# Kernel optimization log

Hardware: AMD Instinct MI355X
Metric: run time of the kernel (lower is better)

## Reference

```python
import jax, jax.numpy as jnp
import numpy as np

N = 50000          # nodes
DEG = 16           # uniform neighbor count (avg_degree)
IN_CH = 128        # node feature dim
TYPE_DIM = 32      # type embedding dim
NUM_TYPES = 8
OUT_CH = 128
F = IN_CH + TYPE_DIM   # SAGEConv input dim = 160
H = F                  # PyG LSTMAggregation: LSTM(in_channels, in_channels)


def setup_inputs() -> dict:
    key = jax.random.key(0)
    ks = jax.random.split(key, 12)
    x = jax.random.normal(ks[0], (N, IN_CH), dtype=jnp.float32)
    node_type_ids = jax.random.randint(ks[1], (N,), 0, NUM_TYPES)
    # each node is destination of exactly DEG edges; dst sorted (PyG lstm aggr requires sorted index)
    dst = jnp.repeat(jnp.arange(N), DEG)
    src = jax.random.randint(ks[2], (N * DEG,), 0, N)
    edge_index = jnp.stack([src, dst])
    emb_table = jax.random.normal(ks[3], (NUM_TYPES, TYPE_DIM), dtype=jnp.float32)
    s = 1.0 / np.sqrt(H)
    W_ih = jax.random.uniform(ks[4], (4 * H, F), minval=-s, maxval=s, dtype=jnp.float32)
    W_hh = jax.random.uniform(ks[5], (4 * H, H), minval=-s, maxval=s, dtype=jnp.float32)
    b_ih = jax.random.uniform(ks[6], (4 * H,), minval=-s, maxval=s, dtype=jnp.float32)
    b_hh = jax.random.uniform(ks[7], (4 * H,), minval=-s, maxval=s, dtype=jnp.float32)
    W_l = jax.random.normal(ks[8], (OUT_CH, F), dtype=jnp.float32) * 0.05  # lin_l (with bias)
    b_l = jnp.zeros((OUT_CH,), jnp.float32)
    W_r = jax.random.normal(ks[9], (OUT_CH, F), dtype=jnp.float32) * 0.05  # lin_r (root, no bias)
    return dict(x=x, node_type_ids=node_type_ids, edge_index=edge_index,
                emb_table=emb_table, W_ih=W_ih, W_hh=W_hh, b_ih=b_ih, b_hh=b_hh,
                W_l=W_l, b_l=b_l, W_r=W_r)


def reference(x, node_type_ids, edge_index, emb_table, W_ih, W_hh, b_ih, b_hh, W_l, b_l, W_r):
    n = x.shape[0]
    # type embedding lookup + concat
    h_in = jnp.concatenate([x, emb_table[node_type_ids]], axis=1)   # [N, F]
    src, dst = edge_index[0], edge_index[1]                          # dst sorted
    E = src.shape[0]
    # dense-batch the neighbor messages per destination (to_dense_batch)
    counts = jax.ops.segment_sum(jnp.ones((E,), jnp.int32), dst, num_segments=n)
    starts = jnp.concatenate([jnp.zeros((1,), jnp.int32), jnp.cumsum(counts)[:-1].astype(jnp.int32)])
    pos = jnp.arange(E, dtype=jnp.int32) - starts[dst]               # slot within each node's row
    dense = jnp.zeros((n, DEG, F), h_in.dtype).at[dst, pos].set(h_in[src])  # [N, DEG, F]

    # LSTM aggregation over neighbor sequence (PyG takes last time-step output)
    def step(carry, x_t):
        hh, cc = carry
        gates = x_t @ W_ih.T + b_ih + hh @ W_hh.T + b_hh
        i, f, g, o = jnp.split(gates, 4, axis=-1)
        cc = jax.nn.sigmoid(f) * cc + jax.nn.sigmoid(i) * jnp.tanh(g)
        hh = jax.nn.sigmoid(o) * jnp.tanh(cc)
        return (hh, cc), None

    h0 = jnp.zeros((n, H), h_in.dtype)
    (h_last, _), _ = jax.lax.scan(step, (h0, h0), dense.transpose(1, 0, 2))  # scan over DEG steps

    # SAGEConv: lin_l(aggregated) + lin_r(root), then ReLU (dropout = identity in eval)
    out = h_last @ W_l.T + b_l + h_in @ W_r.T
    return jax.nn.relu(out)
```

## Files before the change

### kernel.cpp

```cpp
#include <hip/hip_runtime.h>
#include <hip/hip_bf16.h>

#define N_NODES 50000
#define DEG     16
#define IN_CH   128
#define TYPE_DIM 32
#define F_DIM   160
#define H_DIM   160
#define OUT_CH  128
#define NSTEP   16
#define LS      168
#define NRES    7

typedef short  bf16x8 __attribute__((ext_vector_type(8)));
typedef float  f32x4  __attribute__((ext_vector_type(4)));
typedef unsigned int u32x4 __attribute__((ext_vector_type(4)));

__device__ ushort g_hin[N_NODES * F_DIM];
__device__ ushort g_wfrag[400 * 64 * 8];
__device__ ushort g_wlrfrag[80 * 64 * 8];
__device__ float  g_bsum[4 * H_DIM];

static __device__ __forceinline__ ushort f2bf(float v) {
    union { float f; unsigned u; } x; x.f = v;
    unsigned r = x.u + 0x7fff + ((x.u >> 16) & 1);
    return (ushort)(r >> 16);
}
static __device__ __forceinline__ float sigmoid_fast(float x) {
    return __builtin_amdgcn_rcpf(1.f + __expf(-x));
}
static __device__ __forceinline__ float tanh_fast(float x) {
    float e = __expf(2.f * x);
    return 1.f - 2.f * __builtin_amdgcn_rcpf(e + 1.f);
}

__global__ void pack_kernel(const float* __restrict__ Wih, const float* __restrict__ Whh,
                            const float* __restrict__ bih, const float* __restrict__ bhh,
                            const float* __restrict__ Wl,  const float* __restrict__ Wr)
{
    int gid = blockIdx.x * 256 + threadIdx.x;
    if (gid < 400 * 64) {
        int frag = gid >> 6, lane = gid & 63;
        int p = frag & 3, kc = (frag >> 2) % 10, qg = frag / 40;
        int row = p * 160 + qg * 16 + (lane & 15);
        int quad = lane >> 4;
        const float* src; int k0;
        if (kc < 5) { src = Wih + row * 160; k0 = kc * 32 + quad * 8; }
        else        { src = Whh + row * 160; k0 = (kc - 5) * 32 + quad * 8; }
        ushort tmp[8];
        #pragma unroll
        for (int j = 0; j < 8; j++) tmp[j] = f2bf(src[k0 + j]);
        ((u32x4*)g_wfrag)[frag * 64 + lane] = *(const u32x4*)tmp;
    } else if (gid < 400 * 64 + 80 * 64) {
        int g2 = gid - 400 * 64;
        int frag = g2 >> 6, lane = g2 & 63;
        int nt = frag & 7, kc = frag >> 3;
        int row = nt * 16 + (lane & 15);
        int quad = lane >> 4;
        int k0 = kc * 32 + quad * 8;
        ushort tmp[8];
        #pragma unroll
        for (int j = 0; j < 8; j++) {
            int k = k0 + j;
            float v = (k < 160) ? Wl[row * 160 + k] : Wr[row * 160 + (k - 160)];
            tmp[j] = f2bf(v);
        }
        ((u32x4*)g_wlrfrag)[frag * 64 + lane] = *(const u32x4*)tmp;
    } else if (gid < 400 * 64 + 80 * 64 + 640) {
        int i = gid - (400 * 64 + 80 * 64);
        g_bsum[i] = bih[i] + bhh[i];
    }
}

__global__ void build_hin(const float* __restrict__ x, const int* __restrict__ tids,
                          const float* __restrict__ emb)
{
    int i = blockIdx.x * 256 + threadIdx.x;
    if (i >= N_NODES * F_DIM) return;
    int n = i / F_DIM, d = i - n * F_DIM;
    float v = (d < IN_CH) ? x[n * IN_CH + d] : emb[tids[n] * TYPE_DIM + (d - IN_CH)];
    g_hin[i] = f2bf(v);
}

__launch_bounds__(640, 3)
__global__ void lstm_sage_db(const int* __restrict__ edge_src,
                             const float* __restrict__ bl,
                             float* __restrict__ out)
{
    extern __shared__ ushort lds[];
    constexpr int BSZ  = 64 * LS;
    constexpr int XOFF = 0;
    constexpr int HOFF = 2 * BSZ;
    constexpr int WOFF = 4 * BSZ;

    const int tid  = threadIdx.x;
    const int lane = tid & 63;
    const int wv   = tid >> 6;
    const int col  = lane & 15, quad = lane >> 4;
    const int nb   = blockIdx.x * 64;

    float bG4[4];
    #pragma unroll
    for (int p = 0; p < 4; p++) bG4[p] = g_bsum[p * 160 + wv * 16 + col];

    for (int i = tid; i < BSZ; i += 640) lds[HOFF + i] = 0;

    float c_st[4][4];
    #pragma unroll
    for (int m = 0; m < 4; m++)
        #pragma unroll
        for (int r = 0; r < 4; r++) c_st[m][r] = 0.f;

    const int grow  = tid / 10;
    const int gpart = tid - grow * 10;
    const int node_g = nb + grow;
    const int own = (node_g < N_NODES ? node_g : 0);
    const int sbase = own * DEG;

    const u32x4* wq = (const u32x4*)g_wfrag + wv * 40 * 64 + lane;

    {
        u32x4* wl = (u32x4*)(lds + WOFF) + wv * (NRES * 64) + lane;
        #pragma unroll
        for (int f = 0; f < NRES; f++) {
            int kcp = (f < 4) ? (5 * 4 + f) : (6 * 4 + (f - 4));
            wl[f * 64] = wq[kcp * 64];
        }
    }
    const u32x4* wlr = (const u32x4*)(lds + WOFF) + wv * (NRES * 64) + lane;

    {
        int s0 = edge_src[sbase + 0];
        int s1 = edge_src[sbase + 1];
        const u32x4* sp0 = (const u32x4*)(g_hin + s0 * F_DIM);
        const u32x4* sp1 = (const u32x4*)(g_hin + s1 * F_DIM);
        u32x4* d0 = (u32x4*)(lds + XOFF + grow * LS);
        u32x4* d1 = (u32x4*)(lds + XOFF + BSZ + grow * LS);
        d0[gpart]      = sp0[gpart];
        d0[gpart + 10] = sp0[gpart + 10];
        d1[gpart]      = sp1[gpart];
        d1[gpart + 10] = sp1[gpart + 10];
    }
    int snext = edge_src[sbase + 2];

    const int aoff = col * LS + quad * 8;
    const int hoff = quad * 4 * LS + wv * 16 + col;

    __syncthreads();

    f32x4 acc[4][4];
    #pragma unroll
    for (int m = 0; m < 4; m++)
        #pragma unroll
        for (int p = 0; p < 4; p++)
            acc[m][p] = (f32x4){bG4[p], bG4[p], bG4[p], bG4[p]};
    #pragma unroll
    for (int kx = 0; kx < 5; kx++) {
        bf16x8 bfr[4];
        #pragma unroll
        for (int p = 0; p < 4; p++) {
            u32x4 u = wq[(kx * 4 + p) * 64];
            bfr[p] = *(const bf16x8*)&u;
        }
        const ushort* ab = lds + XOFF + kx * 32 + aoff;
        bf16x8 afr[4];
        #pragma unroll
        for (int m = 0; m < 4; m++)
            afr[m] = *(const bf16x8*)(ab + m * (16 * LS));
        #pragma unroll
        for (int m = 0; m < 4; m++)
            #pragma unroll
            for (int p = 0; p < 4; p++)
                acc[m][p] = __builtin_amdgcn_mfma_f32_16x16x32_bf16(
                    afr[m], bfr[p], acc[m][p], 0, 0, 0);
    }

    #pragma unroll 1
    for (int t = 0; t < NSTEP; t++) {
        __syncthreads();
        const int cur = (t & 1) * BSZ, nxt = ((t & 1) ^ 1) * BSZ;

        u32x4 P0, P1;
        if (t < NSTEP - 1) {
            const u32x4* sp = (const u32x4*)(g_hin + ((t < NSTEP - 2) ? snext : own) * F_DIM);
            P0 = sp[gpart];
            P1 = sp[gpart + 10];
            snext = edge_src[sbase + ((t + 3 < DEG) ? t + 3 : 0)];
        }

        const ushort* Hc = lds + HOFF + cur;
        #pragma unroll
        for (int kh = 0; kh < 5; kh++) {
            bf16x8 bfr[4];
            #pragma unroll
            for (int p = 0; p < 4; p++) {
                u32x4 u;
                if (kh == 0)                u = wlr[p * 64];
                else if (kh == 1 && p < 3)  u = wlr[(4 + p) * 64];
                else                        u = wq[((5 + kh) * 4 + p) * 64];
                bfr[p] = *(const bf16x8*)&u;
            }
            const ushort* ab = Hc + kh * 32 + aoff;
            bf16x8 afr[4];
            #pragma unroll
            for (int m = 0; m < 4; m++)
                afr[m] = *(const bf16x8*)(ab + m * (16 * LS));
            #pragma unroll
            for (int m = 0; m < 4; m++)
                #pragma unroll
                for (int p = 0; p < 4; p++)
                    acc[m][p] = __builtin_amdgcn_mfma_f32_16x16x32_bf16(
                        afr[m], bfr[p], acc[m][p], 0, 0, 0);
        }

        ushort* Hn = lds + HOFF + nxt;
        #pragma unroll
        for (int m = 0; m < 4; m++) {
            #pragma unroll
            for (int r = 0; r < 4; r++) {
                float c = sigmoid_fast(acc[m][1][r]) * c_st[m][r]
                        + sigmoid_fast(acc[m][0][r]) * tanh_fast(acc[m][2][r]);
                c_st[m][r] = c;
                float h = sigmoid_fast(acc[m][3][r]) * tanh_fast(c);
                Hn[hoff + (m * 16 + r) * LS] = f2bf(h);
            }
        }

        if (t < NSTEP - 1) {
            {
                u32x4* dp = (u32x4*)(lds + XOFF + cur + grow * LS);
                dp[gpart] = P0; dp[gpart + 10] = P1;
            }
            #pragma unroll
            for (int m = 0; m < 4; m++)
                #pragma unroll
                for (int p = 0; p < 4; p++)
                    acc[m][p] = (f32x4){bG4[p], bG4[p], bG4[p], bG4[p]};
            const ushort* Xn = lds + XOFF + nxt;
            #pragma unroll
            for (int kx = 0; kx < 5; kx++) {
                bf16x8 bfr[4];
                #pragma unroll
                for (int p = 0; p < 4; p++) {
                    u32x4 u = wq[(kx * 4 + p) * 64];
                    bfr[p] = *(const bf16x8*)&u;
                }
                const ushort* ab = Xn + kx * 32 + aoff;
                bf16x8 afr[4];
                #pragma unroll
                for (int m = 0; m < 4; m++)
                    afr[m] = *(const bf16x8*)(ab + m * (16 * LS));
                #pragma unroll
                for (int m = 0; m < 4; m++)
                    #pragma unroll
                    for (int p = 0; p < 4; p++)
                        acc[m][p] = __builtin_amdgcn_mfma_f32_16x16x32_bf16(
                            afr[m], bfr[p], acc[m][p], 0, 0, 0);
            }
        }
    }

    __syncthreads();

    if (wv < 8) {
        const int m = wv & 3, pb = (wv >> 2) * 4;
        f32x4 acc2[4];
        #pragma unroll
        for (int p = 0; p < 4; p++) {
            float b = bl[(pb + p) * 16 + col];
            acc2[p] = (f32x4){b, b, b, b};
        }
        const u32x4* wq2 = (const u32x4*)g_wlrfrag + lane;
        #pragma unroll
        for (int kc = 0; kc < 10; kc++) {
            bf16x8 bfr[4];
            #pragma unroll
            for (int p = 0; p < 4; p++) {
                u32x4 u = wq2[(kc * 8 + pb + p) * 64];
                bfr[p] = *(const bf16x8*)&u;
            }
            const ushort* ab = ((kc < 5) ? (lds + HOFF + kc * 32) : (lds + XOFF + (kc - 5) * 32))
                               + (m * 16 + col) * LS + quad * 8;
            bf16x8 afr = *(const bf16x8*)ab;
            #pragma unroll
            for (int p = 0; p < 4; p++)
                acc2[p] = __builtin_amdgcn_mfma_f32_16x16x32_bf16(afr, bfr[p], acc2[p], 0, 0, 0);
        }
        #pragma unroll
        for (int p = 0; p < 4; p++) {
            int ocol = (pb + p) * 16 + col;
            #pragma unroll
            for (int r = 0; r < 4; r++) {
                int node = nb + m * 16 + quad * 4 + r;
                if (node < N_NODES) {
                    float v = acc2[p][r];
                    out[node * OUT_CH + ocol] = v > 0.f ? v : 0.f;
                }
            }
        }
    }
}

__launch_bounds__(640)
__global__ void lstm_sage_sb(const int* __restrict__ edge_src,
                             const float* __restrict__ bl,
                             float* __restrict__ out)
{
    __shared__ ushort Xb[64 * LS];
    __shared__ ushort Hb[64 * LS];

    const int tid  = threadIdx.x;
    const int lane = tid & 63;
    const int wv   = tid >> 6;
    const int col  = lane & 15, quad = lane >> 4;
    const int nb   = blockIdx.x * 64;

    float bG4[4];
    #pragma unroll
    for (int p = 0; p < 4; p++) bG4[p] = g_bsum[p * 160 + wv * 16 + col];

    for (int i = tid; i < 64 * LS; i += 640) Hb[i] = 0;

    float c_st[4][4];
    #pragma unroll
    for (int m = 0; m < 4; m++)
        #pragma unroll
        for (int r = 0; r < 4; r++) c_st[m][r] = 0.f;

    unsigned hn[4][2];

    const int grow  = tid / 10;
    const int gpart = tid - grow * 10;
    const int node_g = nb + grow;
    const int sbase = (node_g < N_NODES ? node_g : 0) * DEG;

    u32x4 P0, P1;
    {
        int s = edge_src[sbase];
        const u32x4* sp = (const u32x4*)(g_hin + s * F_DIM);
        P0 = sp[gpart]; P1 = sp[gpart + 10];
    }
    int snext = edge_src[sbase + 1];

    #pragma unroll 1
    for (int t = 0; t < NSTEP; t++) {
        if (t > 0) {
            #pragma unroll
            for (int m = 0; m < 4; m++)
                #pragma unroll
                for (int k = 0; k < 2; k++) {
                    int a = (m * 16 + quad * 4 + 2 * k) * LS + wv * 16 + col;
                    unsigned pk = hn[m][k];
                    Hb[a]      = (ushort)pk;
                    Hb[a + LS] = (ushort)(pk >> 16);
                }
        }
        {
            u32x4* dp = (u32x4*)(Xb + grow * LS);
            dp[gpart] = P0; dp[gpart + 10] = P1;
        }
        __syncthreads();

        {
            const u32x4* sp = (t < NSTEP - 1)
                ? (const u32x4*)(g_hin + snext * F_DIM)
                : (const u32x4*)(g_hin + (node_g < N_NODES ? node_g : 0) * F_DIM);
            P0 = sp[gpart]; P1 = sp[gpart + 10];
            snext = edge_src[sbase + ((t + 2 < DEG) ? t + 2 : 0)];
        }

        f32x4 acc[4][4];
        #pragma unroll
        for (int m = 0; m < 4; m++)
            #pragma unroll
            for (int p = 0; p < 4; p++)
                acc[m][p] = (f32x4){bG4[p], bG4[p], bG4[p], bG4[p]};

        const u32x4* wq = (const u32x4*)g_wfrag + wv * 40 * 64 + lane;
        #pragma unroll
        for (int kc = 0; kc < 10; kc++) {
            bf16x8 bfr[4];
            #pragma unroll
            for (int p = 0; p < 4; p++) {
                u32x4 u = wq[(kc * 4 + p) * 64];
                bfr[p] = *(const bf16x8*)&u;
            }
            const ushort* ab = ((kc < 5) ? (Xb + kc * 32) : (Hb + (kc - 5) * 32))
                               + col * LS + quad * 8;
            bf16x8 afr[4];
            #pragma unroll
            for (int m = 0; m < 4; m++)
                afr[m] = *(const bf16x8*)(ab + m * (16 * LS));
            #pragma unroll
            for (int m = 0; m < 4; m++)
                #pragma unroll
                for (int p = 0; p < 4; p++)
                    acc[m][p] = __builtin_amdgcn_mfma_f32_16x16x32_bf16(
                        afr[m], bfr[p], acc[m][p], 0, 0, 0);
        }
        #pragma unroll
        for (int m = 0; m < 4; m++) {
            #pragma unroll
            for (int k = 0; k < 2; k++) {
                unsigned pk = 0;
                #pragma unroll
                for (int h2 = 0; h2 < 2; h2++) {
                    int r = 2 * k + h2;
                    float c = sigmoid_fast(acc[m][1][r]) * c_st[m][r]
                            + sigmoid_fast(acc[m][0][r]) * tanh_fast(acc[m][2][r]);
                    c_st[m][r] = c;
                    float h = sigmoid_fast(acc[m][3][r]) * tanh_fast(c);
                    pk |= ((unsigned)f2bf(h)) << (16 * h2);
                }
                hn[m][k] = pk;
            }
        }
        __syncthreads();
    }

    #pragma unroll
    for (int m = 0; m < 4; m++)
        #pragma unroll
        for (int k = 0; k < 2; k++) {
            int a = (m * 16 + quad * 4 + 2 * k) * LS + wv * 16 + col;
            unsigned pk = hn[m][k];
            Hb[a]      = (ushort)pk;
            Hb[a + LS] = (ushort)(pk >> 16);
        }
    {
        u32x4* dp = (u32x4*)(Xb + grow * LS);
        dp[gpart] = P0; dp[gpart + 10] = P1;
    }
    __syncthreads();

    if (wv < 8) {
        const int m = wv & 3, pb = (wv >> 2) * 4;
        f32x4 acc[4];
        #pragma unroll
        for (int p = 0; p < 4; p++) {
            float b = bl[(pb + p) * 16 + col];
            acc[p] = (f32x4){b, b, b, b};
        }
        const u32x4* wq2 = (const u32x4*)g_wlrfrag + lane;
        #pragma unroll
        for (int kc = 0; kc < 10; kc++) {
            bf16x8 bfr[4];
            #pragma unroll
            for (int p = 0; p < 4; p++) {
                u32x4 u = wq2[(kc * 8 + pb + p) * 64];
                bfr[p] = *(const bf16x8*)&u;
            }
            const ushort* ab = ((kc < 5) ? (Hb + kc * 32) : (Xb + (kc - 5) * 32))
                               + (m * 16 + col) * LS + quad * 8;
            bf16x8 afr = *(const bf16x8*)ab;
            #pragma unroll
            for (int p = 0; p < 4; p++)
                acc[p] = __builtin_amdgcn_mfma_f32_16x16x32_bf16(afr, bfr[p], acc[p], 0, 0, 0);
        }
        #pragma unroll
        for (int p = 0; p < 4; p++) {
            int ocol = (pb + p) * 16 + col;
            #pragma unroll
            for (int r = 0; r < 4; r++) {
                int node = nb + m * 16 + quad * 4 + r;
                if (node < N_NODES) {
                    float v = acc[p][r];
                    out[node * OUT_CH + ocol] = v > 0.f ? v : 0.f;
                }
            }
        }
    }
}

extern "C" void kernel_launch(void* const* d_in, const int* in_sizes, int n_in,
                              void* d_out, int out_size, void* d_ws, size_t ws_size,
                              hipStream_t stream)
{
    const float* x      = (const float*)d_in[0];
    const int*   tids   = (const int*)  d_in[1];
    const int*   esrc   = (const int*)  d_in[2];
    const float* emb    = (const float*)d_in[3];
    const float* Wih    = (const float*)d_in[4];
    const float* Whh    = (const float*)d_in[5];
    const float* bih    = (const float*)d_in[6];
    const float* bhh    = (const float*)d_in[7];
    const float* Wl     = (const float*)d_in[8];
    const float* blin   = (const float*)d_in[9];
    const float* Wr     = (const float*)d_in[10];
    float* out = (float*)d_out;

    hipLaunchKernelGGL(pack_kernel, dim3(123), dim3(256), 0, stream,
                       Wih, Whh, bih, bhh, Wl, Wr);
    hipLaunchKernelGGL(build_hin, dim3((N_NODES * F_DIM + 255) / 256), dim3(256), 0, stream,
                       x, tids, emb);

    const int dbShmem = (4 * 64 * LS + NRES * 10 * 64 * 8) * (int)sizeof(ushort);
    (void)hipFuncSetAttribute((const void*)lstm_sage_db,
                              hipFuncAttributeMaxDynamicSharedMemorySize, dbShmem);
    hipFuncAttributes fa;
    bool dbOk = (hipFuncGetAttributes(&fa, (const void*)lstm_sage_db) == hipSuccess) &&
                (fa.maxDynamicSharedSizeBytes >= dbShmem);

    if (dbOk) {
        hipLaunchKernelGGL(lstm_sage_db, dim3((N_NODES + 63) / 64), dim3(640),
                           dbShmem, stream, esrc, blin, out);
    } else {
        hipLaunchKernelGGL(lstm_sage_sb, dim3((N_NODES + 63) / 64), dim3(640),
                           0, stream, esrc, blin, out);
    }
}
```

Before: 796.0 us.

## Single-buffer X/H tiles and keep eleven W_hh fragments resident in LDS

Drops the double-buffered X and H LDS tiles in favour of single buffers, holding the prefetched neighbor row and packed new hidden state in registers until the next step writes them to LDS. Each step now fuses the input and recurrent GEMMs into one ten-chunk K loop. The LDS freed this way is used to cache eleven W_hh fragments per wave instead of seven, cutting global/L2 weight reloads. In exchange each step needs two barriers and carries more live registers, which may hurt occupancy or overlap.

```diff
diff --git a/kernel.cpp b/kernel.cpp
--- a/kernel.cpp
+++ b/kernel.cpp
@@ -10,7 +10,7 @@
 #define OUT_CH  128
 #define NSTEP   16
 #define LS      168
-#define NRES    7
+#define NRES    11
 
 typedef short  bf16x8 __attribute__((ext_vector_type(8)));
 typedef float  f32x4  __attribute__((ext_vector_type(4)));
@@ -83,15 +83,15 @@
 }
 
 __launch_bounds__(640, 3)
-__global__ void lstm_sage_db(const int* __restrict__ edge_src,
-                             const float* __restrict__ bl,
-                             float* __restrict__ out)
+__global__ void lstm_sage_r11(const int* __restrict__ edge_src,
+                              const float* __restrict__ bl,
+                              float* __restrict__ out)
 {
     extern __shared__ ushort lds[];
     constexpr int BSZ  = 64 * LS;
     constexpr int XOFF = 0;
-    constexpr int HOFF = 2 * BSZ;
-    constexpr int WOFF = 4 * BSZ;
+    constexpr int HOFF = BSZ;
+    constexpr int WOFF = 2 * BSZ;
 
     const int tid  = threadIdx.x;
     const int lane = tid & 63;
@@ -111,6 +111,8 @@
         #pragma unroll
         for (int r = 0; r < 4; r++) c_st[m][r] = 0.f;
 
+    unsigned hn[4][2];
+
     const int grow  = tid / 10;
     const int gpart = tid - grow * 10;
     const int node_g = nb + grow;
@@ -123,84 +125,70 @@
         u32x4* wl = (u32x4*)(lds + WOFF) + wv * (NRES * 64) + lane;
         #pragma unroll
         for (int f = 0; f < NRES; f++) {
-            int kcp = (f < 4) ? (5 * 4 + f) : (6 * 4 + (f - 4));
+            int kcp = (f < 8) ? (5 * 4 + f) : (7 * 4 + (f - 8));
             wl[f * 64] = wq[kcp * 64];
         }
     }
     const u32x4* wlr = (const u32x4*)(lds + WOFF) + wv * (NRES * 64) + lane;
 
+    u32x4 P0, P1;
     {
-        int s0 = edge_src[sbase + 0];
-        int s1 = edge_src[sbase + 1];
-        const u32x4* sp0 = (const u32x4*)(g_hin + s0 * F_DIM);
-        const u32x4* sp1 = (const u32x4*)(g_hin + s1 * F_DIM);
-        u32x4* d0 = (u32x4*)(lds + XOFF + grow * LS);
-        u32x4* d1 = (u32x4*)(lds + XOFF + BSZ + grow * LS);
-        d0[gpart]      = sp0[gpart];
-        d0[gpart + 10] = sp0[gpart + 10];
-        d1[gpart]      = sp1[gpart];
-        d1[gpart + 10] = sp1[gpart + 10];
-    }
-    int snext = edge_src[sbase + 2];
+        int s = edge_src[sbase];
+        const u32x4* sp = (const u32x4*)(g_hin + s * F_DIM);
+        P0 = sp[gpart]; P1 = sp[gpart + 10];
+    }
+    int snext = edge_src[sbase + 1];
 
     const int aoff = col * LS + quad * 8;
-    const int hoff = quad * 4 * LS + wv * 16 + col;
-
-    __syncthreads();
-
-    f32x4 acc[4][4];
-    #pragma unroll
-    for (int m = 0; m < 4; m++)
-        #pragma unroll
-        for (int p = 0; p < 4; p++)
-            acc[m][p] = (f32x4){bG4[p], bG4[p], bG4[p], bG4[p]};
-    #pragma unroll
-    for (int kx = 0; kx < 5; kx++) {
-        bf16x8 bfr[4];
-        #pragma unroll
-        for (int p = 0; p < 4; p++) {
-            u32x4 u = wq[(kx * 4 + p) * 64];
-            bfr[p] = *(const bf16x8*)&u;
-        }
-        const ushort* ab = lds + XOFF + kx * 32 + aoff;
-        bf16x8 afr[4];
-        #pragma unroll
-        for (int m = 0; m < 4; m++)
-            afr[m] = *(const bf16x8*)(ab + m * (16 * LS));
-        #pragma unroll
-        for (int m = 0; m < 4; m++)
-            #pragma unroll
-            for (int p = 0; p < 4; p++)
-                acc[m][p] = __builtin_amdgcn_mfma_f32_16x16x32_bf16(
-                    afr[m], bfr[p], acc[m][p], 0, 0, 0);
-    }
 
     #pragma unroll 1
     for (int t = 0; t < NSTEP; t++) {
+        if (t > 0) {
+            #pragma unroll
+            for (int m = 0; m < 4; m++)
+                #pragma unroll
+                for (int k = 0; k < 2; k++) {
+                    int a = (m * 16 + quad * 4 + 2 * k) * LS + wv * 16 + col;
+                    unsigned pk = hn[m][k];
+                    lds[HOFF + a]      = (ushort)pk;
+                    lds[HOFF + a + LS] = (ushort)(pk >> 16);
+                }
+        }
+        {
+            u32x4* dp = (u32x4*)(lds + XOFF + grow * LS);
+            dp[gpart] = P0; dp[gpart + 10] = P1;
+        }
         __syncthreads();
-        const int cur = (t & 1) * BSZ, nxt = ((t & 1) ^ 1) * BSZ;
-
-        u32x4 P0, P1;
-        if (t < NSTEP - 1) {
-            const u32x4* sp = (const u32x4*)(g_hin + ((t < NSTEP - 2) ? snext : own) * F_DIM);
-            P0 = sp[gpart];
-            P1 = sp[gpart + 10];
-            snext = edge_src[sbase + ((t + 3 < DEG) ? t + 3 : 0)];
-        }
-
-        const ushort* Hc = lds + HOFF + cur;
-        #pragma unroll
-        for (int kh = 0; kh < 5; kh++) {
+
+        {
+            const u32x4* sp = (t < NSTEP - 1)
+                ? (const u32x4*)(g_hin + snext * F_DIM)
+                : (const u32x4*)(g_hin + own * F_DIM);
+            P0 = sp[gpart]; P1 = sp[gpart + 10];
+            snext = edge_src[sbase + ((t + 2 < DEG) ? t + 2 : 0)];
+        }
+
+        f32x4 acc[4][4];
+        #pragma unroll
+        for (int m = 0; m < 4; m++)
+            #pragma unroll
+            for (int p = 0; p < 4; p++)
+                acc[m][p] = (f32x4){bG4[p], bG4[p], bG4[p], bG4[p]};
+
+        #pragma unroll
+        for (int kc = 0; kc < 10; kc++) {
             bf16x8 bfr[4];
             #pragma unroll
             for (int p = 0; p < 4; p++) {
                 u32x4 u;
-                if (kh == 0)                u = wlr[p * 64];
-                else if (kh == 1 && p < 3)  u = wlr[(4 + p) * 64];
-                else                        u = wq[((5 + kh) * 4 + p) * 64];
+                if (kc == 5)               u = wlr[p * 64];
+                else if (kc == 6)          u = wlr[(4 + p) * 64];
+                else if (kc == 7 && p < 3) u = wlr[(8 + p) * 64];
+                else                       u = wq[(kc * 4 + p) * 64];
                 bfr[p] = *(const bf16x8*)&u;
             }
-            const ushort* ab = Hc + kh * 32 + aoff;
+            const ushort* ab = ((kc < 5) ? (lds + XOFF + kc * 32)
+                                         : (lds + HOFF + (kc - 5) * 32)) + aoff;
             bf16x8 afr[4];
             #pragma unroll
             for (int m = 0; m < 4; m++)
@@ -213,53 +201,39 @@
                         afr[m], bfr[p], acc[m][p], 0, 0, 0);
         }
 
-        ushort* Hn = lds + HOFF + nxt;
         #pragma unroll
         for (int m = 0; m < 4; m++) {
             #pragma unroll
-            for (int r = 0; r < 4; r++) {
-                float c = sigmoid_fast(acc[m][1][r]) * c_st[m][r]
-                        + sigmoid_fast(acc[m][0][r]) * tanh_fast(acc[m][2][r]);
-                c_st[m][r] = c;
-                float h = sigmoid_fast(acc[m][3][r]) * tanh_fast(c);
-                Hn[hoff + (m * 16 + r) * LS] = f2bf(h);
-            }
-        }
-
-        if (t < NSTEP - 1) {
-            {
-                u32x4* dp = (u32x4*)(lds + XOFF + cur + grow * LS);
-                dp[gpart] = P0; dp[gpart + 10] = P1;
-            }
-            #pragma unroll
-            for (int m = 0; m < 4; m++)
-                #pragma unroll
-                for (int p = 0; p < 4; p++)
-                    acc[m][p] = (f32x4){bG4[p], bG4[p], bG4[p], bG4[p]};
-            const ushort* Xn = lds + XOFF + nxt;
-            #pragma unroll
-            for (int kx = 0; kx < 5; kx++) {
-                bf16x8 bfr[4];
-                #pragma unroll
-                for (int p = 0; p < 4; p++) {
-                    u32x4 u = wq[(kx * 4 + p) * 64];
-                    bfr[p] = *(const bf16x8*)&u;
-                }
-                const ushort* ab = Xn + kx * 32 + aoff;
-                bf16x8 afr[4];
-                #pragma unroll
-                for (int m = 0; m < 4; m++)
-                    afr[m] = *(const bf16x8*)(ab + m * (16 * LS));
-                #pragma unroll
-                for (int m = 0; m < 4; m++)
-                    #pragma unroll
-                    for (int p = 0; p < 4; p++)
-                        acc[m][p] = __builtin_amdgcn_mfma_f32_16x16x32_bf16(
-                            afr[m], bfr[p], acc[m][p], 0, 0, 0);
-            }
-        }
-    }
-
+            for (int k = 0; k < 2; k++) {
+                unsigned pk = 0;
+                #pragma unroll
+                for (int h2 = 0; h2 < 2; h2++) {
+                    int r = 2 * k + h2;
+                    float c = sigmoid_fast(acc[m][1][r]) * c_st[m][r]
+                            + sigmoid_fast(acc[m][0][r]) * tanh_fast(acc[m][2][r]);
+                    c_st[m][r] = c;
+                    float h = sigmoid_fast(acc[m][3][r]) * tanh_fast(c);
+                    pk |= ((unsigned)f2bf(h)) << (16 * h2);
+                }
+                hn[m][k] = pk;
+            }
+        }
+        __syncthreads();
+    }
+
+    #pragma unroll
+    for (int m = 0; m < 4; m++)
+        #pragma unroll
+        for (int k = 0; k < 2; k++) {
+            int a = (m * 16 + quad * 4 + 2 * k) * LS + wv * 16 + col;
+            unsigned pk = hn[m][k];
+            lds[HOFF + a]      = (ushort)pk;
+            lds[HOFF + a + LS] = (ushort)(pk >> 16);
+        }
+    {
+        u32x4* dp = (u32x4*)(lds + XOFF + grow * LS);
+        dp[gpart] = P0; dp[gpart + 10] = P1;
+    }
     __syncthreads();
 
     if (wv < 8) {
@@ -279,7 +253,8 @@
                 u32x4 u = wq2[(kc * 8 + pb + p) * 64];
                 bfr[p] = *(const bf16x8*)&u;
             }
-            const ushort* ab = ((kc < 5) ? (lds + HOFF + kc * 32) : (lds + XOFF + (kc - 5) * 32))
+            const ushort* ab = ((kc < 5) ? (lds + HOFF + kc * 32)
+                                         : (lds + XOFF + (kc - 5) * 32))
                                + (m * 16 + col) * LS + quad * 8;
             bf16x8 afr = *(const bf16x8*)ab;
             #pragma unroll
@@ -494,15 +469,15 @@
     hipLaunchKernelGGL(build_hin, dim3((N_NODES * F_DIM + 255) / 256), dim3(256), 0, stream,
                        x, tids, emb);
 
-    const int dbShmem = (4 * 64 * LS + NRES * 10 * 64 * 8) * (int)sizeof(ushort);
-    (void)hipFuncSetAttribute((const void*)lstm_sage_db,
+    const int dbShmem = (2 * 64 * LS + NRES * 10 * 64 * 8) * (int)sizeof(ushort);
+    (void)hipFuncSetAttribute((const void*)lstm_sage_r11,
                               hipFuncAttributeMaxDynamicSharedMemorySize, dbShmem);
     hipFuncAttributes fa;
-    bool dbOk = (hipFuncGetAttributes(&fa, (const void*)lstm_sage_db) == hipSuccess) &&
+    bool dbOk = (hipFuncGetAttributes(&fa, (const void*)lstm_sage_r11) == hipSuccess) &&
                 (fa.maxDynamicSharedSizeBytes >= dbShmem);
 
     if (dbOk) {
-        hipLaunchKernelGGL(lstm_sage_db, dim3((N_NODES + 63) / 64), dim3(640),
+        hipLaunchKernelGGL(lstm_sage_r11, dim3((N_NODES + 63) / 64), dim3(640),
                            dbShmem, stream, esrc, blin, out);
     } else {
         hipLaunchKernelGGL(lstm_sage_sb, dim3((N_NODES + 63) / 64), dim3(640),
```

After: 736.0 us, median of 2. 7.5% less time.
